# Optimization experiments

Hardware: AMD Instinct MI355X
Metric: run time of the kernel (lower is better)

## Reference

```python
import jax, jax.numpy as jnp
import numpy as np

NEG_SLOPE = 0.2  # PyG GATConv default negative_slope


def gat_conv(x, src, dst, W, a_src, a_dst, b, N):
    """Single PyG-style GATConv (add_self_loops already applied via src/dst).
    x: [N, F_in], W: [F_in, H*C], a_src/a_dst: [H, C], b: [H*C].
    Returns [N, H*C] (concat=True)."""
    H, C = a_src.shape
    h = (x @ W).reshape(N, H, C)                      # [N,H,C]
    alpha_src = jnp.sum(h * a_src[None], axis=-1)      # [N,H]
    alpha_dst = jnp.sum(h * a_dst[None], axis=-1)      # [N,H]
    e = jax.nn.leaky_relu(alpha_src[src] + alpha_dst[dst], NEG_SLOPE)  # [E,H]
    # numerically stable segment softmax over incoming edges of each dst node
    m = jax.ops.segment_max(e, dst, num_segments=N)    # [N,H]
    m = jnp.where(jnp.isfinite(m), m, 0.0)
    ex = jnp.exp(e - m[dst])                           # [E,H]
    den = jax.ops.segment_sum(ex, dst, num_segments=N) # [N,H]
    alpha = ex / (den[dst] + 1e-16)                    # [E,H]
    out = jax.ops.segment_sum(h[src] * alpha[..., None], dst, num_segments=N)  # [N,H,C]
    return out.reshape(N, H * C) + b


def setup_inputs() -> dict:
    key = jax.random.key(0)
    ks = jax.random.split(key, 9)
    B, N, E = 2, 50000, 800000
    d_model, n_hidden, en_dim, H = 128, 128, 64, 1
    fea_mats = jax.random.normal(ks[0], (B, N, d_model), dtype=jnp.float32)
    edge_index = jax.random.randint(ks[1], (B, 2, E), 0, N, dtype=jnp.int32)
    s1 = 1.0 / np.sqrt(d_model)
    s2 = 1.0 / np.sqrt(n_hidden)
    return {
        "fea_mats": fea_mats,
        "edge_index": edge_index,
        "W1": jax.random.normal(ks[2], (d_model, H * n_hidden), dtype=jnp.float32) * s1,
        "att_src1": jax.random.normal(ks[3], (H, n_hidden), dtype=jnp.float32) * s2,
        "att_dst1": jax.random.normal(ks[4], (H, n_hidden), dtype=jnp.float32) * s2,
        "b1": jnp.zeros((H * n_hidden,), dtype=jnp.float32),
        "W2": jax.random.normal(ks[5], (H * n_hidden, H * en_dim), dtype=jnp.float32) * s2,
        "att_src2": jax.random.normal(ks[6], (H, en_dim), dtype=jnp.float32) / np.sqrt(en_dim),
        "att_dst2": jax.random.normal(ks[7], (H, en_dim), dtype=jnp.float32) / np.sqrt(en_dim),
        "b2": jnp.zeros((H * en_dim,), dtype=jnp.float32),
    }


def reference(fea_mats, edge_index, W1, att_src1, att_dst1, b1, W2, att_src2, att_dst2, b2):
    B, N, _ = fea_mats.shape
    loops = jnp.arange(N, dtype=edge_index.dtype)

    def per_graph(x, ei):
        # PyG GATConv adds self-loops by default
        src = jnp.concatenate([ei[0], loops])
        dst = jnp.concatenate([ei[1], loops])
        h = gat_conv(x, src, dst, W1, att_src1, att_dst1, b1, N)
        h = jax.nn.relu(h)
        h = gat_conv(h, src, dst, W2, att_src2, att_dst2, b2, N)
        return h  # [N, en_dim]

    return jax.vmap(per_graph)(fea_mats, edge_index)  # [B, N, en_dim]
```

## Files before the change

### kernel.cpp

```cpp
#include <hip/hip_runtime.h>

#define NEG_SLOPE 0.2f
static constexpr int BLK = 256;
static constexpr int EPB = 4096;
static constexpr int CAP = 6144;

typedef short bf16x8 __attribute__((ext_vector_type(8)));
typedef float f32x4  __attribute__((ext_vector_type(4)));
typedef unsigned short u16x8 __attribute__((ext_vector_type(8)));
typedef unsigned short u16x4 __attribute__((ext_vector_type(4)));

static inline int cdiv(long a, long b){ return (int)((a + b - 1) / b); }

__device__ __forceinline__ unsigned short f2bf(float f){
    unsigned u = __float_as_uint(f);
    u += 0x7fff + ((u >> 16) & 1);
    return (unsigned short)(u >> 16);
}
__device__ __forceinline__ float bf2f(unsigned short h){
    return __uint_as_float(((unsigned)h) << 16);
}
__device__ __forceinline__ float lrelu(float v){
    return v > 0.f ? v : NEG_SLOPE * v;
}

struct GP {
    const int* src; const int* dst; const float* X;
    int* gcnt; int* gbase; int* ebuf; int* rowptr; int* csrsrc;
    unsigned short* h1b; unsigned short* h2b;
    float *as1, *ad1, *as2, *ad2; float* outp;
};

template<int CO, int CT, bool RELU_IN, bool BF16OUT>
__device__ __forceinline__ void gemm_dev(
    int bid, const float* __restrict__ X,
    const unsigned short* __restrict__ Wt_hi, const unsigned short* __restrict__ Wt_lo,
    const float* __restrict__ avs, const float* __restrict__ avd,
    void* __restrict__ Hout, float* __restrict__ as_out, float* __restrict__ ad_out,
    int N, unsigned short* smem)
{
    constexpr int CHUNKS = CO / (CT * 16);
    constexpr int HWB = CT * 4096;
    int ch, rtb;
    if (CHUNKS == 1){ ch = 0; rtb = bid; } else { ch = bid & 1; rtb = bid >> 1; }
    int c0 = ch * (CT * 16);

    {
        const char* srch = (const char*)(Wt_hi + (size_t)c0 * 128);
        const char* srcl = (const char*)(Wt_lo + (size_t)c0 * 128);
        #pragma unroll
        for (int it = 0; it < CT * 2; ++it){
            int o = (it * 256 + (int)threadIdx.x) * 16;
            const char* sp = (o < HWB) ? (srch + o) : (srcl + (o - HWB));
            u16x8 v = *(const u16x8*)sp;
            int so = o ^ (((o >> 8) & 7) << 4);
            *(u16x8*)((char*)smem + so) = v;
        }
    }
    __syncthreads();

    int wave = threadIdx.x >> 6;
    int lane = threadIdx.x & 63;
    int rt = rtb * 4 + wave;
    if (rt >= (N >> 4)) return;
    int r0 = rt << 4;
    int rl = lane & 15, g = lane >> 4;
    const float* xrow = X + (long)(r0 + rl) * 128 + g * 8;

    f32x4 acc[CT];
    #pragma unroll
    for (int t = 0; t < CT; t++) acc[t] = (f32x4)(0.f);

    int sw = (rl & 7) << 4;
    #pragma unroll
    for (int ks = 0; ks < 4; ks++){
        float4 xa = *(const float4*)(xrow + ks * 32);
        float4 xb = *(const float4*)(xrow + ks * 32 + 4);
        float xv[8] = {xa.x, xa.y, xa.z, xa.w, xb.x, xb.y, xb.z, xb.w};
        bf16x8 xbf;
        #pragma unroll
        for (int j = 0; j < 8; j++){
            float x = xv[j];
            if (RELU_IN) x = fmaxf(x, 0.f);
            xbf[j] = (short)f2bf(x);
        }
        int rbase = rl * 256 + ks * 64 + g * 16;
        #pragma unroll
        for (int t = 0; t < CT; t++){
            bf16x8 wh = *(const bf16x8*)((char*)smem + ((t * 4096 + rbase) ^ sw));
            bf16x8 wl = *(const bf16x8*)((char*)smem + ((HWB + t * 4096 + rbase) ^ sw));
            acc[t] = __builtin_amdgcn_mfma_f32_16x16x32_bf16(wh, xbf, acc[t], 0, 0, 0);
            acc[t] = __builtin_amdgcn_mfma_f32_16x16x32_bf16(wl, xbf, acc[t], 0, 0, 0);
        }
    }

    float ps = 0.f, pd = 0.f;
    #pragma unroll
    for (int t = 0; t < CT; t++){
        int c = c0 + t * 16 + 4 * g;
        float4 vs4 = *(const float4*)(avs + c);
        float4 vd4 = *(const float4*)(avd + c);
        ps += acc[t][0]*vs4.x + acc[t][1]*vs4.y + acc[t][2]*vs4.z + acc[t][3]*vs4.w;
        pd += acc[t][0]*vd4.x + acc[t][1]*vd4.y + acc[t][2]*vd4.z + acc[t][3]*vd4.w;
        long base = (long)(r0 + rl) * CO + c;
        if (BF16OUT){
            u16x4 pk;
            #pragma unroll
            for (int r = 0; r < 4; r++) pk[r] = f2bf(acc[t][r]);
            *(u16x4*)((unsigned short*)Hout + base) = pk;
        } else {
            float4 pv;
            pv.x = acc[t][0]; pv.y = acc[t][1]; pv.z = acc[t][2]; pv.w = acc[t][3];
            *(float4*)((float*)Hout + base) = pv;
        }
    }
    ps += __shfl_xor(ps, 16, 64); ps += __shfl_xor(ps, 32, 64);
    pd += __shfl_xor(pd, 16, 64); pd += __shfl_xor(pd, 32, 64);
    if (g == 0){
        unsafeAtomicAdd(as_out + r0 + rl, ps);
        unsafeAtomicAdd(ad_out + r0 + rl, pd);
    }
}

__device__ __forceinline__ void bucket_dev(
    int bid, const GP* __restrict__ g, int E, int Etot, int nbk, unsigned short* smem)
{
    int* spk   = (int*)smem;
    int* shist = spk + 4096;
    int* sbase = shist + 256;
    int tid = (int)threadIdx.x;
    for (int i = tid; i < nbk; i += 256) shist[i] = 0;
    __syncthreads();
    int e0 = bid * EPB;
    #pragma unroll
    for (int i = 0; i < EPB / 256; i++){
        int idx = i * 256 + tid; int e = e0 + idx;
        unsigned p = 0xFFFFFFFFu;
        if (e < Etot){
            int s, d;
            if (e < E){ s = g->src[e]; d = g->dst[e]; } else { s = e - E; d = s; }
            p = ((unsigned)s << 16) | (unsigned)d;
            atomicAdd(&shist[d >> 8], 1);
        }
        spk[idx] = (int)p;
    }
    __syncthreads();
    for (int i = tid; i < nbk; i += 256){
        sbase[i] = atomicAdd(&g->gcnt[i], shist[i]);
        shist[i] = 0;
    }
    __syncthreads();
    #pragma unroll
    for (int i = 0; i < EPB / 256; i++){
        int idx = i * 256 + tid;
        unsigned p = (unsigned)spk[idx];
        if (p != 0xFFFFFFFFu){
            int d = (int)(p & 0xFFFFu); int b = d >> 8;
            int r = sbase[b] + atomicAdd(&shist[b], 1);
            if (r < CAP) g->ebuf[(size_t)b * CAP + r] = (int)p;
        }
    }
}

__device__ __forceinline__ void fine_dev(int k, const GP* __restrict__ g, int N, int Etot)
{
    __shared__ int pk2[CAP];
    __shared__ int fs[256];
    __shared__ int fill[256];
    __shared__ int fh[256];
    int tid = (int)threadIdx.x;
    int cnt = min(g->gcnt[k], CAP);
    int bb  = g->gbase[k];
    for (int i = tid; i < cnt; i += 256) pk2[i] = g->ebuf[(size_t)k * CAP + i];
    fh[tid] = 0; fill[tid] = 0;
    __syncthreads();
    for (int i = tid; i < cnt; i += 256) atomicAdd(&fh[pk2[i] & 255], 1);
    __syncthreads();
    int v = fh[tid];
    fs[tid] = v;
    __syncthreads();
    #pragma unroll
    for (int off = 1; off < 256; off <<= 1){
        int t = (tid >= off) ? fs[tid - off] : 0;
        __syncthreads();
        fs[tid] += t;
        __syncthreads();
    }
    int excl = fs[tid] - v;
    __syncthreads();
    fs[tid] = excl;
    __syncthreads();
    int node = k * 256 + tid;
    if (node < N) g->rowptr[node] = bb + excl;
    if (k == 0 && tid == 0) g->rowptr[N] = Etot;
    for (int i = tid; i < cnt; i += 256){
        unsigned p = (unsigned)pk2[i];
        int f = (int)(p & 255u);
        int r = atomicAdd(&fill[f], 1);
        g->csrsrc[bb + fs[f] + r] = (int)(p >> 16);
    }
}

template<int CO, int GRP>
__device__ __forceinline__ void agg_core(
    const int* __restrict__ rowptr, const int* __restrict__ csr_src,
    const float* __restrict__ as, const float* __restrict__ ad,
    const unsigned short* __restrict__ hb, int node, int ql, float* acc)
{
    int start = rowptr[node];
    int deg   = rowptr[node + 1] - start;
    float adv = ad[node];

    int sv[4]; float ev[4];
    #pragma unroll
    for (int q = 0; q < 4; q++){
        int idx = q * GRP + ql;
        sv[q] = 0; ev[q] = -1e30f;
        if (idx < deg){ sv[q] = csr_src[start + idx]; ev[q] = lrelu(as[sv[q]] + adv); }
    }
    float m = fmaxf(fmaxf(ev[0], ev[1]), fmaxf(ev[2], ev[3]));
    if (deg > 4 * GRP){
        for (int j = 4 * GRP + ql; j < deg; j += GRP)
            m = fmaxf(m, lrelu(as[csr_src[start + j]] + adv));
    }
    #pragma unroll
    for (int off = GRP >> 1; off; off >>= 1) m = fmaxf(m, __shfl_xor(m, off, GRP));

    float xq[4]; float sum = 0.f;
    #pragma unroll
    for (int q = 0; q < 4; q++){
        xq[q] = (q * GRP + ql < deg) ? __expf(ev[q] - m) : 0.f;
        sum += xq[q];
    }
    if (deg > 4 * GRP){
        for (int j = 4 * GRP + ql; j < deg; j += GRP)
            sum += __expf(lrelu(as[csr_src[start + j]] + adv) - m);
    }
    #pragma unroll
    for (int off = GRP >> 1; off; off >>= 1) sum += __shfl_xor(sum, off, GRP);
    float inv = 1.f / (sum + 1e-16f);

    #pragma unroll
    for (int i = 0; i < 8; i++) acc[i] = 0.f;

    #pragma unroll
    for (int q = 0; q < 4; q++){
        int rem = deg - q * GRP;
        if (rem <= 0) break;
        int lim = rem < GRP ? rem : GRP;
        float aq = xq[q] * inv; int sq = sv[q];
        int t = 0;
        for (; t + 3 < lim; t += 4){
            int   s0 = __shfl(sq, t+0, GRP), s1 = __shfl(sq, t+1, GRP);
            int   s2 = __shfl(sq, t+2, GRP), s3 = __shfl(sq, t+3, GRP);
            float a0 = __shfl(aq, t+0, GRP), a1 = __shfl(aq, t+1, GRP);
            float a2 = __shfl(aq, t+2, GRP), a3 = __shfl(aq, t+3, GRP);
            u16x8 r0 = *(const u16x8*)(hb + (long)s0 * CO + ql * 8);
            u16x8 r1 = *(const u16x8*)(hb + (long)s1 * CO + ql * 8);
            u16x8 r2 = *(const u16x8*)(hb + (long)s2 * CO + ql * 8);
            u16x8 r3 = *(const u16x8*)(hb + (long)s3 * CO + ql * 8);
            #pragma unroll
            for (int i = 0; i < 8; i++)
                acc[i] += a0 * bf2f(r0[i]) + a1 * bf2f(r1[i])
                        + a2 * bf2f(r2[i]) + a3 * bf2f(r3[i]);
        }
        for (; t < lim; t++){
            int   s0 = __shfl(sq, t, GRP);
            float a0 = __shfl(aq, t, GRP);
            u16x8 r0 = *(const u16x8*)(hb + (long)s0 * CO + ql * 8);
            #pragma unroll
            for (int i = 0; i < 8; i++) acc[i] += a0 * bf2f(r0[i]);
        }
        if (lim < GRP) break;
    }
    if (deg > 4 * GRP){
        for (int j = 4 * GRP; j < deg; j++){
            int sj = csr_src[start + j];
            float aj = __expf(lrelu(as[sj] + adv) - m) * inv;
            u16x8 r0 = *(const u16x8*)(hb + (long)sj * CO + ql * 8);
            #pragma unroll
            for (int i = 0; i < 8; i++) acc[i] += aj * bf2f(r0[i]);
        }
    }
}

__global__ __launch_bounds__(BLK) void prep_k(
    const float* __restrict__ W1, const float* __restrict__ W2,
    unsigned short* __restrict__ w1h, unsigned short* __restrict__ w1l,
    unsigned short* __restrict__ w2h, unsigned short* __restrict__ w2l)
{
    int i = blockIdx.x * BLK + threadIdx.x;
    if (i < 128 * 128){
        int c = i >> 7, k = i & 127;
        float w = W1[k * 128 + c];
        unsigned short hi = f2bf(w);
        w1h[i] = hi; w1l[i] = f2bf(w - bf2f(hi));
        if (i < 64 * 128){
            float w2 = W2[k * 64 + c];
            unsigned short hi2 = f2bf(w2);
            w2h[i] = hi2; w2l[i] = f2bf(w2 - bf2f(hi2));
        }
    }
}

__global__ __launch_bounds__(256, 4) void kA(
    GP a, GP b, const unsigned short* __restrict__ w1h, const unsigned short* __restrict__ w1l,
    const float* __restrict__ avs1, const float* __restrict__ avd1,
    int EB_a, int EB_b, int GB_a, int GB_b, int E, int Etot, int N, int nbk)
{
    __shared__ unsigned short smem[16384];
    int bid = blockIdx.x;
    if (bid < EB_a){ bucket_dev(bid, &a, E, Etot, nbk, smem); return; }
    bid -= EB_a;
    if (bid < EB_b){ bucket_dev(bid, &b, E, Etot, nbk, smem); return; }
    bid -= EB_b;
    if (bid < GB_a){ gemm_dev<128,4,false,true>(bid, a.X, w1h, w1l, avs1, avd1, a.h1b, a.as1, a.ad1, N, smem); return; }
    bid -= GB_a;
    if (bid < GB_b) gemm_dev<128,4,false,true>(bid, b.X, w1h, w1l, avs1, avd1, b.h1b, b.as1, b.ad1, N, smem);
}

__global__ __launch_bounds__(256) void kscan(GP a, GP b, int nbk){
    const GP* g = (blockIdx.x == 0) ? &a : &b;
    __shared__ int sh[256];
    int tid = (int)threadIdx.x;
    int v = (tid < nbk) ? g->gcnt[tid] : 0;
    sh[tid] = v;
    __syncthreads();
    #pragma unroll
    for (int off = 1; off < 256; off <<= 1){
        int t = (tid >= off) ? sh[tid - off] : 0;
        __syncthreads();
        sh[tid] += t;
        __syncthreads();
    }
    if (tid < nbk) g->gbase[tid] = sh[tid] - v;
}

__global__ __launch_bounds__(256) void kB(GP a, GP b, int nb_a, int nb_b, int N, int Etot){
    int bid = blockIdx.x; const GP* g; int k;
    if (bid < nb_a){ g = &a; k = bid; }
    else { k = bid - nb_a; if (k >= nb_b) return; g = &b; }
    fine_dev(k, g, N, Etot);
}

__global__ __launch_bounds__(BLK) void agg1f_k(
    GP a, GP b, const float* __restrict__ b1,
    const unsigned short* __restrict__ w2h, const unsigned short* __restrict__ w2l,
    const float* __restrict__ avs2, const float* __restrict__ avd2,
    int AB_a, int AB_b, int N)
{
    __shared__ unsigned short xlds[16 * 128];
    int bid = blockIdx.x; const GP* g;
    if (bid < AB_a){ g = &a; }
    else { bid -= AB_a; if (bid >= AB_b) return; g = &b; }
    int tid = (int)threadIdx.x;
    int grp = tid >> 4, ql = tid & 15;
    int node = bid * 16 + grp;

    {
        u16x8 xv;
        if (node < N){
            float acc[8];
            agg_core<128,16>(g->rowptr, g->csrsrc, g->as1, g->ad1, g->h1b, node, ql, acc);
            #pragma unroll
            for (int i = 0; i < 8; i++)
                xv[i] = f2bf(fmaxf(acc[i] + b1[ql * 8 + i], 0.f));
        } else {
            #pragma unroll
            for (int i = 0; i < 8; i++) xv[i] = 0;
        }
        int bo = (grp * 256 + ql * 16) ^ ((grp & 7) << 4);
        *(u16x8*)((char*)xlds + bo) = xv;
    }
    __syncthreads();

    int lane = tid & 63, wv = tid >> 6;
    int rl = lane & 15, kg = lane >> 4;
    f32x4 d = (f32x4)(0.f);
    #pragma unroll
    for (int kb = 0; kb < 4; kb++){
        bf16x8 af = *(const bf16x8*)((char*)xlds + ((rl * 256 + kb * 64 + kg * 16) ^ ((rl & 7) << 4)));
        long wo = (long)(wv * 16 + rl) * 128 + kb * 32 + kg * 8;
        bf16x8 bh = *(const bf16x8*)(w2h + wo);
        bf16x8 bl = *(const bf16x8*)(w2l + wo);
        d = __builtin_amdgcn_mfma_f32_16x16x32_bf16(af, bh, d, 0, 0, 0);
        d = __builtin_amdgcn_mfma_f32_16x16x32_bf16(af, bl, d, 0, 0, 0);
    }
    float pvs = avs2[wv * 16 + rl], pvd = avd2[wv * 16 + rl];
    #pragma unroll
    for (int reg = 0; reg < 4; reg++){
        int nd = bid * 16 + 4 * kg + reg;
        float hv = d[reg];
        if (nd < N) g->h2b[(long)nd * 64 + wv * 16 + rl] = f2bf(hv);
        float s_ = hv * pvs, d_ = hv * pvd;
        #pragma unroll
        for (int off = 1; off < 16; off <<= 1){
            s_ += __shfl_xor(s_, off, 16);
            d_ += __shfl_xor(d_, off, 16);
        }
        if (rl == 0 && nd < N){
            unsafeAtomicAdd(g->as2 + nd, s_);
            unsafeAtomicAdd(g->ad2 + nd, d_);
        }
    }
}

__global__ __launch_bounds__(BLK) void agg2f_k(
    GP a, GP b, const float* __restrict__ bias, int AB_a, int AB_b, int N)
{
    int bid = blockIdx.x; const GP* g;
    if (bid < AB_a){ g = &a; }
    else { bid -= AB_a; if (bid >= AB_b) return; g = &b; }
    int tid = (int)threadIdx.x;
    int grp = tid >> 3, ql = tid & 7;
    int node = bid * 32 + grp;
    if (node >= N) return;
    float acc[8];
    agg_core<64,8>(g->rowptr, g->csrsrc, g->as2, g->ad2, g->h2b, node, ql, acc);
    float* o = g->outp + (long)node * 64 + ql * 8;
    #pragma unroll
    for (int i = 0; i < 8; i += 4){
        float4 ov;
        ov.x = acc[i+0] + bias[ql * 8 + i + 0];
        ov.y = acc[i+1] + bias[ql * 8 + i + 1];
        ov.z = acc[i+2] + bias[ql * 8 + i + 2];
        ov.w = acc[i+3] + bias[ql * 8 + i + 3];
        *(float4*)(o + i) = ov;
    }
}

extern "C" void kernel_launch(void* const* d_in, const int* in_sizes, int n_in,
                              void* d_out, int out_size, void* d_ws, size_t ws_size,
                              hipStream_t stream)
{
    const float* fea  = (const float*)d_in[0];
    const int*   ei   = (const int*)  d_in[1];
    const float* W1   = (const float*)d_in[2];
    const float* av_s1= (const float*)d_in[3];
    const float* av_d1= (const float*)d_in[4];
    const float* b1   = (const float*)d_in[5];
    const float* W2   = (const float*)d_in[6];
    const float* av_s2= (const float*)d_in[7];
    const float* av_d2= (const float*)d_in[8];
    const float* b2   = (const float*)d_in[9];
    float* out = (float*)d_out;

    const int B = 2;
    const int N = out_size / (B * 64);
    const int E = in_sizes[1] / (2 * B);
    const int Etot = E + N;
    const int nbk = (N + 255) >> 8;

    size_t pg = 256 + (size_t)nbk * CAP + (size_t)(N + 2) + (size_t)Etot
              + (size_t)N * (64 + 32);
    size_t wtf = 8192 + 8192 + 4096 + 4096;
    auto total_f = [&](int ng){ return wtf + (size_t)ng * (4 * (size_t)N + 256) + (size_t)ng * pg + 64; };
    bool fused = (ws_size >= total_f(2) * sizeof(float));
    int NG = fused ? 2 : 1;

    float* ws = (float*)d_ws;
    size_t off = 0;
    unsigned short* w1h = (unsigned short*)(ws + off); off += 8192;
    unsigned short* w1l = (unsigned short*)(ws + off); off += 8192;
    unsigned short* w2h = (unsigned short*)(ws + off); off += 4096;
    unsigned short* w2l = (unsigned short*)(ws + off); off += 4096;

    float* zbase = ws + off;
    size_t znum = (size_t)NG * (4 * (size_t)N + 256);
    off += znum;

    GP g[2];
    for (int gi = 0; gi < NG; gi++){
        GP p;
        p.as1  = zbase + (size_t)gi * (4 * (size_t)N + 256);
        p.ad1  = p.as1 + N;
        p.as2  = p.ad1 + N;
        p.ad2  = p.as2 + N;
        p.gcnt = (int*)(p.ad2 + N);
        p.gbase  = (int*)(ws + off); off += 256;
        p.ebuf   = (int*)(ws + off); off += (size_t)nbk * CAP;
        p.rowptr = (int*)(ws + off); off += (size_t)(N + 2);
        p.csrsrc = (int*)(ws + off); off += Etot;
        p.h1b  = (unsigned short*)(ws + off); off += (size_t)N * 64;
        p.h2b  = (unsigned short*)(ws + off); off += (size_t)N * 32;
        g[gi] = p;
    }

    const int RT  = N >> 4;
    const int GB1 = cdiv(RT, 4) * 2;
    const int EBk = cdiv(Etot, EPB);
    const int AB1 = cdiv(N, 16);
    const int AB2 = cdiv(N, 32);

    if (fused){
        for (int bi = 0; bi < 2; bi++){
            g[bi].src = ei + (size_t)bi * 2 * E;
            g[bi].dst = g[bi].src + E;
            g[bi].X   = fea + (size_t)bi * N * 128;
            g[bi].outp= out + (size_t)bi * N * 64;
        }
        hipMemsetAsync(zbase, 0, znum * sizeof(float), stream);
        prep_k<<<cdiv(128*128, BLK), BLK, 0, stream>>>(W1, W2, w1h, w1l, w2h, w2l);
        kA<<<2*EBk + 2*GB1, 256, 0, stream>>>(g[0], g[1], w1h, w1l, av_s1, av_d1,
                                              EBk, EBk, GB1, GB1, E, Etot, N, nbk);
        kscan<<<2, 256, 0, stream>>>(g[0], g[1], nbk);
        kB<<<2*nbk, 256, 0, stream>>>(g[0], g[1], nbk, nbk, N, Etot);
        agg1f_k<<<2*AB1, BLK, 0, stream>>>(g[0], g[1], b1, w2h, w2l, av_s2, av_d2, AB1, AB1, N);
        agg2f_k<<<2*AB2, BLK, 0, stream>>>(g[0], g[1], b2, AB2, AB2, N);
    } else {
        prep_k<<<cdiv(128*128, BLK), BLK, 0, stream>>>(W1, W2, w1h, w1l, w2h, w2l);
        for (int bi = 0; bi < B; bi++){
            GP p = g[0];
            p.src = ei + (size_t)bi * 2 * E;
            p.dst = p.src + E;
            p.X   = fea + (size_t)bi * N * 128;
            p.outp= out + (size_t)bi * N * 64;
            hipMemsetAsync(zbase, 0, znum * sizeof(float), stream);
            kA<<<EBk + GB1, 256, 0, stream>>>(p, p, w1h, w1l, av_s1, av_d1,
                                              EBk, 0, GB1, 0, E, Etot, N, nbk);
            kscan<<<1, 256, 0, stream>>>(p, p, nbk);
            kB<<<nbk, 256, 0, stream>>>(p, p, nbk, 0, N, Etot);
            agg1f_k<<<AB1, BLK, 0, stream>>>(p, p, b1, w2h, w2l, av_s2, av_d2, AB1, 0, N);
            agg2f_k<<<AB2, BLK, 0, stream>>>(p, p, b2, AB2, 0, N);
        }
    }
}
```

Baseline: 204.2 us.

## Process two row tiles per wave in GEMM and layer-1 aggregation blocks

The first-layer GEMM now has each wave compute two 16-row tiles, so each LDS-staged W fragment is reused across twice as many rows and the per-block W staging cost is amortized over half as many blocks. The agg1f kernel likewise handles 32 nodes per block in two halves, reusing the W2 loads and the block setup. This raises register pressure and halves the grid size, which may reduce occupancy and latency hiding in the gather-heavy aggregation.

```diff
diff --git a/kernel.cpp b/kernel.cpp
--- a/kernel.cpp
+++ b/kernel.cpp
@@ -61,64 +61,79 @@
 
     int wave = threadIdx.x >> 6;
     int lane = threadIdx.x & 63;
-    int rt = rtb * 4 + wave;
-    if (rt >= (N >> 4)) return;
-    int r0 = rt << 4;
+    int RTt = N >> 4;
+    int rt0 = rtb * 8 + wave;
+    int rt1 = rt0 + 4;
+    if (rt0 >= RTt) return;
+    bool vB = rt1 < RTt;
     int rl = lane & 15, g = lane >> 4;
-    const float* xrow = X + (long)(r0 + rl) * 128 + g * 8;
-
-    f32x4 acc[CT];
-    #pragma unroll
-    for (int t = 0; t < CT; t++) acc[t] = (f32x4)(0.f);
+    const float* xrowA = X + (long)(rt0 * 16 + rl) * 128 + g * 8;
+    const float* xrowB = X + (long)((vB ? rt1 : rt0) * 16 + rl) * 128 + g * 8;
+
+    f32x4 accA[CT], accB[CT];
+    #pragma unroll
+    for (int t = 0; t < CT; t++){ accA[t] = (f32x4)(0.f); accB[t] = (f32x4)(0.f); }
 
     int sw = (rl & 7) << 4;
     #pragma unroll
     for (int ks = 0; ks < 4; ks++){
-        float4 xa = *(const float4*)(xrow + ks * 32);
-        float4 xb = *(const float4*)(xrow + ks * 32 + 4);
-        float xv[8] = {xa.x, xa.y, xa.z, xa.w, xb.x, xb.y, xb.z, xb.w};
-        bf16x8 xbf;
+        float4 xaA = *(const float4*)(xrowA + ks * 32);
+        float4 xbA = *(const float4*)(xrowA + ks * 32 + 4);
+        float4 xaB = *(const float4*)(xrowB + ks * 32);
+        float4 xbB = *(const float4*)(xrowB + ks * 32 + 4);
+        float xvA[8] = {xaA.x, xaA.y, xaA.z, xaA.w, xbA.x, xbA.y, xbA.z, xbA.w};
+        float xvB[8] = {xaB.x, xaB.y, xaB.z, xaB.w, xbB.x, xbB.y, xbB.z, xbB.w};
+        bf16x8 xbfA, xbfB;
         #pragma unroll
         for (int j = 0; j < 8; j++){
-            float x = xv[j];
-            if (RELU_IN) x = fmaxf(x, 0.f);
-            xbf[j] = (short)f2bf(x);
+            float xA = xvA[j], xB = xvB[j];
+            if (RELU_IN){ xA = fmaxf(xA, 0.f); xB = fmaxf(xB, 0.f); }
+            xbfA[j] = (short)f2bf(xA);
+            xbfB[j] = (short)f2bf(xB);
         }
         int rbase = rl * 256 + ks * 64 + g * 16;
         #pragma unroll
         for (int t = 0; t < CT; t++){
             bf16x8 wh = *(const bf16x8*)((char*)smem + ((t * 4096 + rbase) ^ sw));
             bf16x8 wl = *(const bf16x8*)((char*)smem + ((HWB + t * 4096 + rbase) ^ sw));
-            acc[t] = __builtin_amdgcn_mfma_f32_16x16x32_bf16(wh, xbf, acc[t], 0, 0, 0);
-            acc[t] = __builtin_amdgcn_mfma_f32_16x16x32_bf16(wl, xbf, acc[t], 0, 0, 0);
-        }
-    }
-
-    float ps = 0.f, pd = 0.f;
-    #pragma unroll
-    for (int t = 0; t < CT; t++){
-        int c = c0 + t * 16 + 4 * g;
-        float4 vs4 = *(const float4*)(avs + c);
-        float4 vd4 = *(const float4*)(avd + c);
-        ps += acc[t][0]*vs4.x + acc[t][1]*vs4.y + acc[t][2]*vs4.z + acc[t][3]*vs4.w;
-        pd += acc[t][0]*vd4.x + acc[t][1]*vd4.y + acc[t][2]*vd4.z + acc[t][3]*vd4.w;
-        long base = (long)(r0 + rl) * CO + c;
-        if (BF16OUT){
-            u16x4 pk;
-            #pragma unroll
-            for (int r = 0; r < 4; r++) pk[r] = f2bf(acc[t][r]);
-            *(u16x4*)((unsigned short*)Hout + base) = pk;
-        } else {
-            float4 pv;
-            pv.x = acc[t][0]; pv.y = acc[t][1]; pv.z = acc[t][2]; pv.w = acc[t][3];
-            *(float4*)((float*)Hout + base) = pv;
-        }
-    }
-    ps += __shfl_xor(ps, 16, 64); ps += __shfl_xor(ps, 32, 64);
-    pd += __shfl_xor(pd, 16, 64); pd += __shfl_xor(pd, 32, 64);
-    if (g == 0){
-        unsafeAtomicAdd(as_out + r0 + rl, ps);
-        unsafeAtomicAdd(ad_out + r0 + rl, pd);
+            accA[t] = __builtin_amdgcn_mfma_f32_16x16x32_bf16(wh, xbfA, accA[t], 0, 0, 0);
+            accB[t] = __builtin_amdgcn_mfma_f32_16x16x32_bf16(wh, xbfB, accB[t], 0, 0, 0);
+            accA[t] = __builtin_amdgcn_mfma_f32_16x16x32_bf16(wl, xbfA, accA[t], 0, 0, 0);
+            accB[t] = __builtin_amdgcn_mfma_f32_16x16x32_bf16(wl, xbfB, accB[t], 0, 0, 0);
+        }
+    }
+
+    #pragma unroll
+    for (int half = 0; half < 2; half++){
+        if (half == 1 && !vB) break;
+        int r0 = (half == 0 ? rt0 : rt1) << 4;
+        f32x4* acc = (half == 0) ? accA : accB;
+        float ps = 0.f, pd = 0.f;
+        #pragma unroll
+        for (int t = 0; t < CT; t++){
+            int c = c0 + t * 16 + 4 * g;
+            float4 vs4 = *(const float4*)(avs + c);
+            float4 vd4 = *(const float4*)(avd + c);
+            ps += acc[t][0]*vs4.x + acc[t][1]*vs4.y + acc[t][2]*vs4.z + acc[t][3]*vs4.w;
+            pd += acc[t][0]*vd4.x + acc[t][1]*vd4.y + acc[t][2]*vd4.z + acc[t][3]*vd4.w;
+            long base = (long)(r0 + rl) * CO + c;
+            if (BF16OUT){
+                u16x4 pk;
+                #pragma unroll
+                for (int r = 0; r < 4; r++) pk[r] = f2bf(acc[t][r]);
+                *(u16x4*)((unsigned short*)Hout + base) = pk;
+            } else {
+                float4 pv;
+                pv.x = acc[t][0]; pv.y = acc[t][1]; pv.z = acc[t][2]; pv.w = acc[t][3];
+                *(float4*)((float*)Hout + base) = pv;
+            }
+        }
+        ps += __shfl_xor(ps, 16, 64); ps += __shfl_xor(ps, 32, 64);
+        pd += __shfl_xor(pd, 16, 64); pd += __shfl_xor(pd, 32, 64);
+        if (g == 0){
+            unsafeAtomicAdd(as_out + r0 + rl, ps);
+            unsafeAtomicAdd(ad_out + r0 + rl, pd);
+        }
     }
 }
 
@@ -349,15 +364,16 @@
     const float* __restrict__ avs2, const float* __restrict__ avd2,
     int AB_a, int AB_b, int N)
 {
-    __shared__ unsigned short xlds[16 * 128];
+    __shared__ unsigned short xlds[32 * 128];
     int bid = blockIdx.x; const GP* g;
     if (bid < AB_a){ g = &a; }
     else { bid -= AB_a; if (bid >= AB_b) return; g = &b; }
     int tid = (int)threadIdx.x;
     int grp = tid >> 4, ql = tid & 15;
-    int node = bid * 16 + grp;
-
-    {
+
+    #pragma unroll
+    for (int h = 0; h < 2; h++){
+        int node = bid * 32 + h * 16 + grp;
         u16x8 xv;
         if (node < N){
             float acc[8];
@@ -369,38 +385,43 @@
             #pragma unroll
             for (int i = 0; i < 8; i++) xv[i] = 0;
         }
-        int bo = (grp * 256 + ql * 16) ^ ((grp & 7) << 4);
+        int row = h * 16 + grp;
+        int bo = (row * 256 + ql * 16) ^ ((row & 7) << 4);
         *(u16x8*)((char*)xlds + bo) = xv;
     }
     __syncthreads();
 
     int lane = tid & 63, wv = tid >> 6;
     int rl = lane & 15, kg = lane >> 4;
-    f32x4 d = (f32x4)(0.f);
-    #pragma unroll
-    for (int kb = 0; kb < 4; kb++){
-        bf16x8 af = *(const bf16x8*)((char*)xlds + ((rl * 256 + kb * 64 + kg * 16) ^ ((rl & 7) << 4)));
-        long wo = (long)(wv * 16 + rl) * 128 + kb * 32 + kg * 8;
-        bf16x8 bh = *(const bf16x8*)(w2h + wo);
-        bf16x8 bl = *(const bf16x8*)(w2l + wo);
-        d = __builtin_amdgcn_mfma_f32_16x16x32_bf16(af, bh, d, 0, 0, 0);
-        d = __builtin_amdgcn_mfma_f32_16x16x32_bf16(af, bl, d, 0, 0, 0);
-    }
     float pvs = avs2[wv * 16 + rl], pvd = avd2[wv * 16 + rl];
     #pragma unroll
-    for (int reg = 0; reg < 4; reg++){
-        int nd = bid * 16 + 4 * kg + reg;
-        float hv = d[reg];
-        if (nd < N) g->h2b[(long)nd * 64 + wv * 16 + rl] = f2bf(hv);
-        float s_ = hv * pvs, d_ = hv * pvd;
+    for (int h = 0; h < 2; h++){
+        f32x4 d = (f32x4)(0.f);
         #pragma unroll
-        for (int off = 1; off < 16; off <<= 1){
-            s_ += __shfl_xor(s_, off, 16);
-            d_ += __shfl_xor(d_, off, 16);
-        }
-        if (rl == 0 && nd < N){
-            unsafeAtomicAdd(g->as2 + nd, s_);
-            unsafeAtomicAdd(g->ad2 + nd, d_);
+        for (int kb = 0; kb < 4; kb++){
+            int row = h * 16 + rl;
+            bf16x8 af = *(const bf16x8*)((char*)xlds + ((row * 256 + kb * 64 + kg * 16) ^ ((row & 7) << 4)));
+            long wo = (long)(wv * 16 + rl) * 128 + kb * 32 + kg * 8;
+            bf16x8 bh = *(const bf16x8*)(w2h + wo);
+            bf16x8 bl = *(const bf16x8*)(w2l + wo);
+            d = __builtin_amdgcn_mfma_f32_16x16x32_bf16(af, bh, d, 0, 0, 0);
+            d = __builtin_amdgcn_mfma_f32_16x16x32_bf16(af, bl, d, 0, 0, 0);
+        }
+        #pragma unroll
+        for (int reg = 0; reg < 4; reg++){
+            int nd = bid * 32 + h * 16 + 4 * kg + reg;
+            float hv = d[reg];
+            if (nd < N) g->h2b[(long)nd * 64 + wv * 16 + rl] = f2bf(hv);
+            float s_ = hv * pvs, d_ = hv * pvd;
+            #pragma unroll
+            for (int off = 1; off < 16; off <<= 1){
+                s_ += __shfl_xor(s_, off, 16);
+                d_ += __shfl_xor(d_, off, 16);
+            }
+            if (rl == 0 && nd < N){
+                unsafeAtomicAdd(g->as2 + nd, s_);
+                unsafeAtomicAdd(g->ad2 + nd, d_);
+            }
         }
     }
 }
@@ -487,9 +508,9 @@
     }
 
     const int RT  = N >> 4;
-    const int GB1 = cdiv(RT, 4) * 2;
+    const int GB1 = cdiv(RT, 8) * 2;
     const int EBk = cdiv(Etot, EPB);
-    const int AB1 = cdiv(N, 16);
+    const int AB1 = cdiv(N, 32);
     const int AB2 = cdiv(N, 32);
 
     if (fused){
```

Result: no change. 202.9 us (-0.7%).
